# Kernel optimization log

Measured on AMD Instinct MI355X. Metric: run time of the kernel, lower is better.

## Reference

```python
import jax, jax.numpy as jnp
import numpy as np

WINDOW = 128  # crop size (compute_crops default window_size)


def centre_crop(centroids, window_size, h, w):
    # centroids: [C,2] int; returns flat gather coords [2, C*ws*ws]
    half = window_size // 2
    cy = jnp.clip(centroids[:, 0], half, h - half)
    cx = jnp.clip(centroids[:, 1], half, w - half)
    gy, gx = jnp.meshgrid(jnp.arange(window_size), jnp.arange(window_size), indexing='ij')
    rows = (cy - half)[:, None, None] + gy[None]  # [C,ws,ws]
    cols = (cx - half)[:, None, None] + gx[None]
    return jnp.stack([rows.reshape(-1), cols.reshape(-1)])  # [2, C*ws*ws]


def setup_inputs() -> dict:
    key = jax.random.key(0)
    ks = jax.random.split(key, 8)
    E, S, C, H, W = 6, 1, 512, 1024, 1024
    Dh = 16
    return {
        'x': jax.random.normal(ks[0], (E, H, W), dtype=jnp.float32),
        'sigma': jax.random.uniform(ks[1], (S, H, W), dtype=jnp.float32),
        'c': jax.random.normal(ks[2], (C, E), dtype=jnp.float32),
        'W1': jax.random.normal(ks[3], (E + S, Dh), dtype=jnp.float32) * 0.3,
        'b1': jnp.zeros((Dh,), dtype=jnp.float32),
        'W2': jax.random.normal(ks[4], (Dh, Dh), dtype=jnp.float32) * 0.3,
        'b2': jnp.zeros((Dh,), dtype=jnp.float32),
        'W3': jax.random.normal(ks[5], (Dh, 1), dtype=jnp.float32) * 0.3,
        'b3': jnp.zeros((1,), dtype=jnp.float32),
        'centroids_idx': jax.random.randint(ks[6], (C, 2), 0, H, dtype=jnp.int32),
    }


def reference(x, sigma, c, W1, b1, W2, b2, W3, b3, centroids_idx):
    E, h, w = x.shape
    S = sigma.shape[0]
    C = c.shape[0]
    ws = WINDOW
    mesh = centre_crop(centroids_idx, ws, h, w)  # [2, C*ws*ws]
    # gather per-instance windows from concatenated embedding+sigma maps
    xs = jnp.concatenate([x, sigma], axis=0)  # [E+S, H, W]
    g = xs[:, mesh[0], mesh[1]]               # [E+S, C*ws*ws]
    g = g.reshape(E + S, C, ws, ws).transpose(1, 0, 2, 3)  # [C, E+S, ws, ws]
    # subtract centroid descriptor from embedding channels (feature_engineering '0')
    g = jnp.concatenate([g[:, :E] - c[:, :, None, None], g[:, E:]], axis=1)
    feats = g.transpose(0, 2, 3, 1).reshape(-1, E + S)  # [(C*ws*ws), E+S]
    # per-pixel probability MLP (ProbabilityNet)
    hdn = jax.nn.relu(feats @ W1 + b1)
    hdn = jax.nn.relu(hdn @ W2 + b2)
    prob = jax.nn.sigmoid(hdn @ W3 + b3)
    prob = prob.reshape(C, 1, ws, ws)
    # instance-id / coordinate table for the downstream scatter (iidd)
    inst = jnp.repeat(jnp.arange(C, dtype=mesh.dtype), ws * ws)
    iidd = jnp.concatenate([inst[None], mesh], axis=0)  # [3, C*ws*ws]
    return prob, iidd
```

## Files before the change

kernel.cpp:

```cpp
#include <hip/hip_runtime.h>

#define WS 128
#define HW (1024 * 1024)
#define PLANE 8388608

typedef _Float16 half4 __attribute__((ext_vector_type(4)));
typedef _Float16 half8 __attribute__((ext_vector_type(8)));
typedef float floatx4 __attribute__((ext_vector_type(4)));

__global__ __launch_bounds__(256) void precompute_P(
    const float* __restrict__ x,
    const float* __restrict__ sigma,
    const float* __restrict__ W1,
    _Float16* __restrict__ P)
{
    const int px = blockIdx.x * 256 + threadIdx.x;
    float g[7];
#pragma unroll
    for (int e = 0; e < 6; ++e) g[e] = x[e * HW + px];
    g[6] = sigma[px];

    half8 lo, hi;
#pragma unroll
    for (int j = 0; j < 16; ++j) {
        float a = 0.0f;
#pragma unroll
        for (int e = 0; e < 7; ++e)
            a = fmaf(g[e], W1[e * 16 + j], a);
        if (j < 8) lo[j] = (_Float16)a; else hi[j - 8] = (_Float16)a;
    }
    *(half8*)(P + (size_t)px * 16)     = lo;
    *(half8*)(P + (size_t)px * 16 + 8) = hi;
}

__global__ __launch_bounds__(256) void instanseg_mlp(
    const _Float16* __restrict__ P,
    const float* __restrict__ c,
    const float* __restrict__ W1,
    const float* __restrict__ b1,
    const float* __restrict__ W2,
    const float* __restrict__ b2,
    const float* __restrict__ W3,
    const float* __restrict__ b3,
    const int*   __restrict__ cent,
    float* __restrict__ out)
{
    const int cid  = blockIdx.y;
    const int lane = threadIdx.x & 63;
    const int wave = threadIdx.x >> 6;
    const int quad = lane >> 4;
    const int sub  = lane & 15;

    const int cy = min(max(cent[2 * cid], 64), 960);
    const int cx = min(max(cent[2 * cid + 1], 64), 960);
    const int cy0 = cy - 64, cx0 = cx - 64;

    half4 a2;
    float w3f[4], bb2[4];
    half4 qh;
#pragma unroll
    for (int i = 0; i < 4; ++i) {
        const int k = 4 * quad + i;
        a2[i]  = (_Float16)W2[k * 16 + sub];
        w3f[i] = W3[k];
        bb2[i] = b2[k];
        float qv = -b1[k];
#pragma unroll
        for (int e = 0; e < 6; ++e)
            qv = fmaf(W1[e * 16 + k], c[cid * 6 + e], qv);
        qh[i] = (_Float16)qv;
    }
    const float b3v = b3[0];
    const floatx4 zero = {0.0f, 0.0f, 0.0f, 0.0f};

    const int wavestart = blockIdx.x * 2048 + wave * 512;

    for (int it = 0; it < 8; ++it) {
        const int start = wavestart + it * 64;
        float logit[4];
#pragma unroll
        for (int ch = 0; ch < 4; ++ch) {
            const int gp  = start + ch * 16 + sub;
            const int src = (cy0 + (gp >> 7)) * 1024 + cx0 + (gp & 127);

            half4 v = *(const half4*)(P + (size_t)src * 16 + quad * 4);
            half4 h = v - qh;
#pragma unroll
            for (int i = 0; i < 4; ++i)
                h[i] = h[i] > (_Float16)0.0f ? h[i] : (_Float16)0.0f;

            floatx4 c2 = __builtin_amdgcn_mfma_f32_16x16x16f16(a2, h, zero, 0, 0, 0);

            float part = 0.0f;
#pragma unroll
            for (int i = 0; i < 4; ++i)
                part = fmaf(w3f[i], fmaxf(c2[i] + bb2[i], 0.0f), part);
            part += __shfl_xor(part, 16, 64);
            part += __shfl_xor(part, 32, 64);
            logit[ch] = part;
        }

        const float l01 = (quad & 1) ? logit[1] : logit[0];
        const float l23 = (quad & 1) ? logit[3] : logit[2];
        const float lg  = (quad & 2) ? l23 : l01;
        const float prob = 1.0f / (1.0f + __expf(-(lg + b3v)));

        const int gps = start + lane;
        const int n   = cid * 16384 + gps;
        out[n]             = prob;
        out[PLANE + n]     = (float)cid;
        out[2 * PLANE + n] = (float)(cy0 + (gps >> 7));
        out[3 * PLANE + n] = (float)(cx0 + (gps & 127));
    }
}

extern "C" void kernel_launch(void* const* d_in, const int* in_sizes, int n_in,
                              void* d_out, int out_size, void* d_ws, size_t ws_size,
                              hipStream_t stream) {
    const float* x     = (const float*)d_in[0];
    const float* sigma = (const float*)d_in[1];
    const float* c     = (const float*)d_in[2];
    const float* W1    = (const float*)d_in[3];
    const float* b1    = (const float*)d_in[4];
    const float* W2    = (const float*)d_in[5];
    const float* b2    = (const float*)d_in[6];
    const float* W3    = (const float*)d_in[7];
    const float* b3    = (const float*)d_in[8];
    const int*   cent  = (const int*)d_in[9];
    float* out = (float*)d_out;
    _Float16* P = (_Float16*)d_ws;

    precompute_P<<<dim3(HW / 256), dim3(256), 0, stream>>>(x, sigma, W1, P);
    instanseg_mlp<<<dim3(8, 512), dim3(256), 0, stream>>>(
        P, c, W1, b1, W2, b2, W3, b3, cent, out);
}
```

Baseline: 208.5 us.

## Move index-table writes into prep kernel with vectorized float4 stores

The three iidd planes (instance id, row, col) are now written by extra blocks of the prep kernel using float4 stores, instead of by scalar stores inside the MLP kernel. The MLP kernel only stores the probability plane. It also hoists the gather address computation, unrolls the loop by two, and uses a hardware reciprocal in the sigmoid. The aim is to cut store instruction count and overlap the index writes with the P precompute. The cost is that the prep kernel gets larger and the two block types have unbalanced work.

```diff
diff --git a/kernel.cpp b/kernel.cpp
--- a/kernel.cpp
+++ b/kernel.cpp
@@ -1,6 +1,5 @@
 #include <hip/hip_runtime.h>
 
-#define WS 128
 #define HW (1024 * 1024)
 #define PLANE 8388608
 
@@ -8,29 +7,53 @@
 typedef _Float16 half8 __attribute__((ext_vector_type(8)));
 typedef float floatx4 __attribute__((ext_vector_type(4)));
 
-__global__ __launch_bounds__(256) void precompute_P(
+__global__ __launch_bounds__(256) void prep(
     const float* __restrict__ x,
     const float* __restrict__ sigma,
     const float* __restrict__ W1,
-    _Float16* __restrict__ P)
+    const int*   __restrict__ cent,
+    _Float16* __restrict__ P,
+    float* __restrict__ out)
 {
-    const int px = blockIdx.x * 256 + threadIdx.x;
-    float g[7];
+    if (blockIdx.x < 4096) {
+        const int px = blockIdx.x * 256 + threadIdx.x;
+        float g[7];
 #pragma unroll
-    for (int e = 0; e < 6; ++e) g[e] = x[e * HW + px];
-    g[6] = sigma[px];
+        for (int e = 0; e < 6; ++e) g[e] = x[e * HW + px];
+        g[6] = sigma[px];
 
-    half8 lo, hi;
+        half8 lo, hi;
 #pragma unroll
-    for (int j = 0; j < 16; ++j) {
-        float a = 0.0f;
+        for (int j = 0; j < 16; ++j) {
+            float a = 0.0f;
 #pragma unroll
-        for (int e = 0; e < 7; ++e)
-            a = fmaf(g[e], W1[e * 16 + j], a);
-        if (j < 8) lo[j] = (_Float16)a; else hi[j - 8] = (_Float16)a;
+            for (int e = 0; e < 7; ++e)
+                a = fmaf(g[e], W1[e * 16 + j], a);
+            if (j < 8) lo[j] = (_Float16)a; else hi[j - 8] = (_Float16)a;
+        }
+        *(half8*)(P + (size_t)px * 16)     = lo;
+        *(half8*)(P + (size_t)px * 16 + 8) = hi;
+    } else {
+        const int b   = blockIdx.x - 4096;
+        const int w   = b >> 2;
+        const int qtr = b & 3;
+        const int cy0 = min(max(cent[2 * w], 64), 960) - 64;
+        const int cx0 = min(max(cent[2 * w + 1], 64), 960) - 64;
+        const float iw = (float)w;
+#pragma unroll
+        for (int pass = 0; pass < 4; ++pass) {
+            const int p = qtr * 4096 + pass * 1024 + threadIdx.x * 4;
+            const int n = w * 16384 + p;
+            const float row = (float)(cy0 + (p >> 7));
+            const float c0  = (float)(cx0 + (p & 127));
+            float4 iv = {iw, iw, iw, iw};
+            float4 rv = {row, row, row, row};
+            float4 cv = {c0, c0 + 1.0f, c0 + 2.0f, c0 + 3.0f};
+            *(float4*)(out + PLANE + n)     = iv;
+            *(float4*)(out + 2 * PLANE + n) = rv;
+            *(float4*)(out + 3 * PLANE + n) = cv;
+        }
     }
-    *(half8*)(P + (size_t)px * 16)     = lo;
-    *(half8*)(P + (size_t)px * 16 + 8) = hi;
 }
 
 __global__ __launch_bounds__(256) void instanseg_mlp(
@@ -51,13 +74,11 @@
     const int quad = lane >> 4;
     const int sub  = lane & 15;
 
-    const int cy = min(max(cent[2 * cid], 64), 960);
-    const int cx = min(max(cent[2 * cid + 1], 64), 960);
-    const int cy0 = cy - 64, cx0 = cx - 64;
+    const int cy0 = min(max(cent[2 * cid], 64), 960) - 64;
+    const int cx0 = min(max(cent[2 * cid + 1], 64), 960) - 64;
 
-    half4 a2;
+    half4 a2, qh;
     float w3f[4], bb2[4];
-    half4 qh;
 #pragma unroll
     for (int i = 0; i < 4; ++i) {
         const int k = 4 * quad + i;
@@ -72,18 +93,18 @@
     }
     const float b3v = b3[0];
     const floatx4 zero = {0.0f, 0.0f, 0.0f, 0.0f};
-
     const int wavestart = blockIdx.x * 2048 + wave * 512;
 
+#pragma unroll 2
     for (int it = 0; it < 8; ++it) {
         const int start = wavestart + it * 64;
+        const int srcbase = (cy0 + (start >> 7)) * 1024 + cx0 + (start & 127);
+        const _Float16* pb = P + (size_t)(srcbase + sub) * 16 + quad * 4;
+
         float logit[4];
 #pragma unroll
         for (int ch = 0; ch < 4; ++ch) {
-            const int gp  = start + ch * 16 + sub;
-            const int src = (cy0 + (gp >> 7)) * 1024 + cx0 + (gp & 127);
-
-            half4 v = *(const half4*)(P + (size_t)src * 16 + quad * 4);
+            half4 v = *(const half4*)(pb + ch * 256);
             half4 h = v - qh;
 #pragma unroll
             for (int i = 0; i < 4; ++i)
@@ -103,14 +124,9 @@
         const float l01 = (quad & 1) ? logit[1] : logit[0];
         const float l23 = (quad & 1) ? logit[3] : logit[2];
         const float lg  = (quad & 2) ? l23 : l01;
-        const float prob = 1.0f / (1.0f + __expf(-(lg + b3v)));
+        const float prob = __builtin_amdgcn_rcpf(1.0f + __expf(-(lg + b3v)));
 
-        const int gps = start + lane;
-        const int n   = cid * 16384 + gps;
-        out[n]             = prob;
-        out[PLANE + n]     = (float)cid;
-        out[2 * PLANE + n] = (float)(cy0 + (gps >> 7));
-        out[3 * PLANE + n] = (float)(cx0 + (gps & 127));
+        out[cid * 16384 + start + lane] = prob;
     }
 }
 
@@ -130,7 +146,7 @@
     float* out = (float*)d_out;
     _Float16* P = (_Float16*)d_ws;
 
-    precompute_P<<<dim3(HW / 256), dim3(256), 0, stream>>>(x, sigma, W1, P);
+    prep<<<dim3(4096 + 2048), dim3(256), 0, stream>>>(x, sigma, W1, cent, P, out);
     instanseg_mlp<<<dim3(8, 512), dim3(256), 0, stream>>>(
         P, c, W1, b1, W2, b2, W3, b3, cent, out);
 }
```

Result: no change. 209.2 us (+0.3%).
